# Kernel optimization log

Measured on AMD Instinct MI355X. Metric: run time of the kernel, lower is better.

The kernel has to match this reference:

```python
import jax, jax.numpy as jnp
import numpy as np

NUM_GROUPS = 8
EPS = 1e-5


def group_norm(x, gamma, beta):
    # x: [B, C, H, W]
    B, C, H, W = x.shape
    xg = x.reshape(B, NUM_GROUPS, C // NUM_GROUPS, H, W)
    mean = xg.mean(axis=(2, 3, 4), keepdims=True)
    var = xg.var(axis=(2, 3, 4), keepdims=True)
    xn = ((xg - mean) * jax.lax.rsqrt(var + EPS)).reshape(B, C, H, W)
    return xn * gamma[None, :, None, None] + beta[None, :, None, None]


def conv1x1(x, w, b):
    # x: [B, C, H, W], w: [Cout, Cin], b: [Cout]
    return jnp.einsum('bchw,oc->bohw', x, w) + b[None, :, None, None]


def setup_inputs() -> dict:
    key = jax.random.key(0)
    ks = jax.random.split(key, 7)
    C = 128
    x = jax.random.normal(ks[0], (4, C, 64, 64), dtype=jnp.float32)
    norm_w = jnp.ones((C,), dtype=jnp.float32)
    norm_b = jnp.zeros((C,), dtype=jnp.float32)
    s = 1.0 / np.sqrt(C)
    qkv_w = jax.random.normal(ks[1], (3 * C, C), dtype=jnp.float32) * s
    qkv_b = jax.random.normal(ks[2], (3 * C,), dtype=jnp.float32) * 0.01
    proj_w = jax.random.normal(ks[3], (C, C), dtype=jnp.float32) * s
    proj_b = jax.random.normal(ks[4], (C,), dtype=jnp.float32) * 0.01
    return {"x": x, "norm_w": norm_w, "norm_b": norm_b,
            "qkv_w": qkv_w, "qkv_b": qkv_b,
            "proj_w": proj_w, "proj_b": proj_b}


def reference(x, norm_w, norm_b, qkv_w, qkv_b, proj_w, proj_b):
    B, C, H, W = x.shape
    qkv = conv1x1(group_norm(x, norm_w, norm_b), qkv_w, qkv_b)
    q, k, v = jnp.split(qkv, 3, axis=1)           # each [B, C, H, W]
    q = q.reshape(B, C, H * W).transpose(0, 2, 1)  # [B, HW, C]
    k = k.reshape(B, C, H * W)                     # [B, C, HW]
    v = v.reshape(B, C, H * W).transpose(0, 2, 1)  # [B, HW, C]
    scale = 1.0 / np.sqrt(C).astype(np.float32)
    attn = jax.nn.softmax(jnp.einsum('bnc,bcm->bnm', q, k) * scale, axis=-1)
    out = jnp.einsum('bnm,bmc->bnc', attn, v)      # [B, HW, C]
    out = out.transpose(0, 2, 1).reshape(B, C, H, W)
    return x + conv1x1(out, proj_w, proj_b)
```

## Files before the change

kernel.cpp:

```cpp
#include <hip/hip_runtime.h>

typedef unsigned short u16;
typedef unsigned int   u32;

#define HW 4096
#define NC 128

typedef __bf16 bf16x8 __attribute__((ext_vector_type(8)));
typedef float  f32x16 __attribute__((ext_vector_type(16)));

__device__ __forceinline__ bf16x8 as_bf8(uint4 u){
    union { uint4 u; bf16x8 b; } c; c.u = u; return c.b;
}
__device__ __forceinline__ u16 f2bf(float f){
    u32 u = __float_as_uint(f);
    return (u16)((u + 0x7fffu + ((u >> 16) & 1u)) >> 16);
}
__device__ __forceinline__ u32 pack2(float a, float b){
    return ((__float_as_uint(a) + 0x8000u) >> 16) | ((__float_as_uint(b) + 0x8000u) & 0xffff0000u);
}
__device__ __forceinline__ float bf_lo(u32 u){ return __uint_as_float(u << 16); }
__device__ __forceinline__ float bf_hi(u32 u){ return __uint_as_float(u & 0xffff0000u); }
__device__ __forceinline__ void unpack8(uint4 u, float* v){
    v[0]=bf_lo(u.x); v[1]=bf_hi(u.x); v[2]=bf_lo(u.y); v[3]=bf_hi(u.y);
    v[4]=bf_lo(u.z); v[5]=bf_hi(u.z); v[6]=bf_lo(u.w); v[7]=bf_hi(u.w);
}

#define GLOAD_LDS16(g, l) \
    __builtin_amdgcn_global_load_lds((const __attribute__((address_space(1))) u32*)(const void*)(g), \
                                     (__attribute__((address_space(3))) u32*)(void*)(l), 16, 0, 0)

__global__ __launch_bounds__(256) void gn_stats_kernel(const float* __restrict__ x,
                                                       float* __restrict__ stats){
    int bg = blockIdx.x >> 3, part = blockIdx.x & 7;
    const float4* p = (const float4*)(x + (size_t)bg * 65536 + part * 8192);
    float s = 0.f, ss = 0.f;
    #pragma unroll
    for (int i = 0; i < 8; i++){
        float4 u = p[threadIdx.x + i*256];
        s  += u.x + u.y + u.z + u.w;
        ss += u.x*u.x + u.y*u.y + u.z*u.z + u.w*u.w;
    }
    #pragma unroll
    for (int off = 32; off > 0; off >>= 1){
        s  += __shfl_xor(s,  off);
        ss += __shfl_xor(ss, off);
    }
    __shared__ float rs[4], rss[4];
    int wid = threadIdx.x >> 6;
    if ((threadIdx.x & 63) == 0){ rs[wid] = s; rss[wid] = ss; }
    __syncthreads();
    if (threadIdx.x == 0){
        stats[bg*16 + part*2]     = rs[0]+rs[1]+rs[2]+rs[3];
        stats[bg*16 + part*2 + 1] = rss[0]+rss[1]+rss[2]+rss[3];
    }
}

__global__ __launch_bounds__(256) void wprep_kernel(const float* __restrict__ qkv_w,
                                                    const float* __restrict__ proj_w,
                                                    uint4* __restrict__ Wf,
                                                    uint4* __restrict__ Pf){
    int id = blockIdx.x*256 + threadIdx.x;
    const float* src; uint4* dst; int fi;
    if (id < 6144){ src = qkv_w; dst = Wf; fi = id; }
    else          { src = proj_w; dst = Pf; fi = id - 6144; }
    int l = fi & 63, ks = (fi >> 6) & 7, ob = fi >> 9;
    int o = ob*32 + (l & 31);
    int c = ks*16 + ((l >> 5) << 3);
    const float* s = src + o*128 + c;
    dst[fi] = make_uint4(pack2(s[0],s[1]), pack2(s[2],s[3]), pack2(s[4],s[5]), pack2(s[6],s[7]));
}

__global__ __launch_bounds__(256) void qkv_kernel(const float* __restrict__ x,
                                                  const float* __restrict__ stats,
                                                  const float* __restrict__ gamma,
                                                  const float* __restrict__ beta,
                                                  const uint4* __restrict__ Wf,
                                                  const float* __restrict__ bias,
                                                  uint4* __restrict__ Qf,
                                                  uint4* __restrict__ Kf,
                                                  uint4* __restrict__ Vf){
    __shared__ float gaL[128], beL[128], biasL[384];
    int b = blockIdx.x >> 7, tokblk = blockIdx.x & 127;
    int t = threadIdx.x, lane = t & 63, wv = t >> 6;
    if (t < 128){
        int g = t >> 4;
        float S = 0.f, SS = 0.f;
        #pragma unroll
        for (int p = 0; p < 8; p++){
            S  += stats[(b*8 + g)*16 + p*2];
            SS += stats[(b*8 + g)*16 + p*2 + 1];
        }
        float mean = S * (1.f/65536.f);
        float rstd = rsqrtf(SS * (1.f/65536.f) - mean*mean + 1e-5f);
        float ga = gamma[t] * rstd;
        gaL[t] = ga; beL[t] = beta[t] - mean*ga;
    }
    if (t < 192){ biasL[t] = bias[t]; biasL[t+192] = bias[t+192]; }
    __syncthreads();

    int h = lane >> 5, tl = lane & 31;
    uint4 xf[8];
    const float* xb = x + (size_t)b*128*HW + tokblk*32 + tl;
    #pragma unroll
    for (int ks = 0; ks < 8; ks++){
        int c0 = ks*16 + h*8;
        float4 g0 = *(float4*)&gaL[c0], g1 = *(float4*)&gaL[c0+4];
        float4 e0 = *(float4*)&beL[c0], e1 = *(float4*)&beL[c0+4];
        float v[8];
        #pragma unroll
        for (int j = 0; j < 8; j++) v[j] = xb[(size_t)(c0+j)*HW];
        v[0] = fmaf(v[0], g0.x, e0.x); v[1] = fmaf(v[1], g0.y, e0.y);
        v[2] = fmaf(v[2], g0.z, e0.z); v[3] = fmaf(v[3], g0.w, e0.w);
        v[4] = fmaf(v[4], g1.x, e1.x); v[5] = fmaf(v[5], g1.y, e1.y);
        v[6] = fmaf(v[6], g1.z, e1.z); v[7] = fmaf(v[7], g1.w, e1.w);
        xf[ks] = make_uint4(pack2(v[0],v[1]), pack2(v[2],v[3]), pack2(v[4],v[5]), pack2(v[6],v[7]));
    }

    bool up = (lane >= 32);
    #pragma unroll
    for (int i = 0; i < 3; i++){
        int ob = wv*3 + i;
        uint4 wf[8];
        #pragma unroll
        for (int ks = 0; ks < 8; ks++) wf[ks] = Wf[(ob*8 + ks)*64 + lane];
        f32x16 D;
        #pragma unroll
        for (int r = 0; r < 16; r++) D[r] = 0.f;
        if (ob < 8){
            #pragma unroll
            for (int ks = 0; ks < 8; ks++)
                D = __builtin_amdgcn_mfma_f32_32x32x16_bf16(as_bf8(wf[ks]), as_bf8(xf[ks]), D, 0,0,0);
            #pragma unroll
            for (int r = 0; r < 16; r++)
                D[r] += biasL[ob*32 + (r&3) + 8*(r>>2) + 4*h];
            u32 pk[8], xch[8];
            #pragma unroll
            for (int j = 0; j < 8; j++) pk[j] = pack2(D[2*j], D[2*j+1]);
            #pragma unroll
            for (int j = 0; j < 8; j++) xch[j] = __shfl_xor(pk[j], 32);
            uint4 F0 = up ? make_uint4(xch[2],xch[3],pk[2],pk[3]) : make_uint4(pk[0],pk[1],xch[0],xch[1]);
            uint4 F1 = up ? make_uint4(xch[6],xch[7],pk[6],pk[7]) : make_uint4(pk[4],pk[5],xch[4],xch[5]);
            uint4* dst = (ob < 4) ? Qf : Kf;
            int obl = ob & 3;
            size_t base = (((size_t)b*128 + tokblk)*8 + obl*2)*64 + lane;
            dst[base] = F0; dst[base + 64] = F1;
        } else {
            #pragma unroll
            for (int ks = 0; ks < 8; ks++)
                D = __builtin_amdgcn_mfma_f32_32x32x16_bf16(as_bf8(xf[ks]), as_bf8(wf[ks]), D, 0,0,0);
            int nb = ob - 8;
            float vb = biasL[256 + nb*32 + tl];
            #pragma unroll
            for (int r = 0; r < 16; r++) D[r] += vb;
            u32 pk[8], xch[8];
            #pragma unroll
            for (int j = 0; j < 8; j++) pk[j] = pack2(D[2*j], D[2*j+1]);
            #pragma unroll
            for (int j = 0; j < 8; j++) xch[j] = __shfl_xor(pk[j], 32);
            uint4 F0 = up ? make_uint4(xch[2],xch[3],pk[2],pk[3]) : make_uint4(pk[0],pk[1],xch[0],xch[1]);
            uint4 F1 = up ? make_uint4(xch[6],xch[7],pk[6],pk[7]) : make_uint4(pk[4],pk[5],xch[4],xch[5]);
            int it = tokblk >> 1, t2 = tokblk & 1;
            size_t base = ((((size_t)b*64 + it)*4 + nb)*4 + t2*2)*64 + lane;
            Vf[base] = F0; Vf[base + 64] = F1;
        }
    }
}

__global__ __launch_bounds__(256, 2) void attn_kernel(const uint4* __restrict__ Qf,
                                                      const uint4* __restrict__ Kf,
                                                      const uint4* __restrict__ Vf,
                                                      u16* __restrict__ Opart,
                                                      float* __restrict__ lsum){
    __shared__ uint4 smem[4096];
    int pair = blockIdx.x & 7, qx = blockIdx.x >> 3;
    int b = pair >> 1, ksp = pair & 1;
    int t = threadIdx.x, lane = t & 63, wv = t >> 6;
    int qh = wv >> 1, kh = wv & 1;
    const float SC = 0.08838834764831845f;

    uint4 qf[8];
    const uint4* qptr = Qf + ((size_t)b*128 + qx*2 + qh)*512 + lane;
    #pragma unroll
    for (int ks = 0; ks < 8; ks++) qf[ks] = qptr[ks*64];

    f32x16 O0, O1, O2, O3;
    #pragma unroll
    for (int r = 0; r < 16; r++){ O0[r]=0.f; O1[r]=0.f; O2[r]=0.f; O3[r]=0.f; }
    float l_i = 0.f;

    const uint4* kg = Kf + ((size_t)b*128 + ksp*64)*512;
    const uint4* vg = Vf + ((size_t)b*64  + ksp*32)*1024;

    #pragma unroll
    for (int i = 0; i < 4; i++){
        GLOAD_LDS16(kg + t + i*256, &smem[t + i*256]);
        GLOAD_LDS16(vg + t + i*256, &smem[2048 + t + i*256]);
    }
    __syncthreads();

    for (int it = 0; it < 32; it++){
        int cur = it & 1;
        if (it < 31){
            const uint4* kg2 = kg + (it+1)*1024;
            const uint4* vg2 = vg + (it+1)*1024;
            #pragma unroll
            for (int i = 0; i < 4; i++){
                GLOAD_LDS16(kg2 + t + i*256, &smem[(cur^1)*1024 + t + i*256]);
                GLOAD_LDS16(vg2 + t + i*256, &smem[2048 + (cur^1)*1024 + t + i*256]);
            }
        }

        f32x16 S0;
        #pragma unroll
        for (int r = 0; r < 16; r++) S0[r] = 0.f;
        #pragma unroll
        for (int ks = 0; ks < 8; ks++)
            S0 = __builtin_amdgcn_mfma_f32_32x32x16_bf16(
                     as_bf8(smem[cur*1024 + ((kh*8 + ks)<<6) + lane]),
                     as_bf8(qf[ks]), S0, 0,0,0);

        float psum = 0.f;
        u32 pk[8];
        #pragma unroll
        for (int q = 0; q < 4; q++){
            float e0 = __expf(__fmaf_rn(S0[q*4+0], SC, -8.f));
            float e1 = __expf(__fmaf_rn(S0[q*4+1], SC, -8.f));
            float e2 = __expf(__fmaf_rn(S0[q*4+2], SC, -8.f));
            float e3 = __expf(__fmaf_rn(S0[q*4+3], SC, -8.f));
            psum += (e0+e1)+(e2+e3);
            pk[2*q] = pack2(e0,e1); pk[2*q+1] = pack2(e2,e3);
        }
        psum += __shfl_xor(psum, 32);
        l_i += psum;

        u32 xch[8];
        #pragma unroll
        for (int i = 0; i < 8; i++) xch[i] = __shfl_xor(pk[i], 32);
        bool up = (lane >= 32);
        uint4 fr0 = up ? make_uint4(xch[2],xch[3],pk[2],pk[3]) : make_uint4(pk[0],pk[1],xch[0],xch[1]);
        uint4 fr1 = up ? make_uint4(xch[6],xch[7],pk[6],pk[7]) : make_uint4(pk[4],pk[5],xch[4],xch[5]);

        int vb = 2048 + cur*1024 + (kh<<7);
        #pragma unroll
        for (int ks = 0; ks < 2; ks++){
            bf16x8 pa = as_bf8(ks ? fr1 : fr0);
            O0 = __builtin_amdgcn_mfma_f32_32x32x16_bf16(pa, as_bf8(smem[vb +   0 + (ks<<6) + lane]), O0, 0,0,0);
            O1 = __builtin_amdgcn_mfma_f32_32x32x16_bf16(pa, as_bf8(smem[vb + 256 + (ks<<6) + lane]), O1, 0,0,0);
            O2 = __builtin_amdgcn_mfma_f32_32x32x16_bf16(pa, as_bf8(smem[vb + 512 + (ks<<6) + lane]), O2, 0,0,0);
            O3 = __builtin_amdgcn_mfma_f32_32x32x16_bf16(pa, as_bf8(smem[vb + 768 + (ks<<6) + lane]), O3, 0,0,0);
        }
        __syncthreads();
    }

    float* fsm  = (float*)smem;
    float* lred = fsm + 8192;
    if (kh == 1){
        #pragma unroll
        for (int r = 0; r < 16; r++){
            fsm[((qh*4+0)*16 + r)*64 + lane] = O0[r];
            fsm[((qh*4+1)*16 + r)*64 + lane] = O1[r];
            fsm[((qh*4+2)*16 + r)*64 + lane] = O2[r];
            fsm[((qh*4+3)*16 + r)*64 + lane] = O3[r];
        }
        if (lane < 32) lred[qh*32 + lane] = l_i;
    }
    __syncthreads();
    if (kh == 0){
        float lt = l_i + lred[qh*32 + (lane & 31)];
        if (lane < 32) lsum[((size_t)(ksp*4 + b))*HW + qx*64 + qh*32 + lane] = lt;
        u16* ob = Opart + (((size_t)(ksp*4 + b))*HW + qx*64 + qh*32)*NC;
        #pragma unroll
        for (int r = 0; r < 16; r++){
            int qr = (r&3) + 8*(r>>2) + 4*(lane>>5);
            int c  = lane & 31;
            ob[qr*NC +      c] = f2bf(O0[r] + fsm[((qh*4+0)*16 + r)*64 + lane]);
            ob[qr*NC + 32 + c] = f2bf(O1[r] + fsm[((qh*4+1)*16 + r)*64 + lane]);
            ob[qr*NC + 64 + c] = f2bf(O2[r] + fsm[((qh*4+2)*16 + r)*64 + lane]);
            ob[qr*NC + 96 + c] = f2bf(O3[r] + fsm[((qh*4+3)*16 + r)*64 + lane]);
        }
    }
}

__global__ __launch_bounds__(256) void combine_kernel(const u16* __restrict__ Op,
                                                      const float* __restrict__ lsum,
                                                      uint4* __restrict__ ao){
    int idx = blockIdx.x*256 + threadIdx.x;
    int row = idx >> 4, cg = idx & 15;
    float inv = 1.f / (lsum[row] + lsum[16384 + row]);
    uint4 u0 = *(const uint4*)(Op + (size_t)row*NC + cg*8);
    uint4 u1 = *(const uint4*)(Op + (size_t)2097152 + (size_t)row*NC + cg*8);
    float v0[8], v1[8];
    unpack8(u0, v0); unpack8(u1, v1);
    u32 pk[4];
    #pragma unroll
    for (int j = 0; j < 4; j++){
        float r0 = (v0[2*j]   + v1[2*j])   * inv;
        float r1 = (v0[2*j+1] + v1[2*j+1]) * inv;
        pk[j] = pack2(r0, r1);
    }
    size_t fi = (((size_t)(row >> 5))*8 + (cg >> 1))*64 + (row & 31) + ((cg & 1) << 5);
    ao[fi] = make_uint4(pk[0], pk[1], pk[2], pk[3]);
}

__global__ __launch_bounds__(256) void proj_kernel(const uint4* __restrict__ aof,
                                                   const uint4* __restrict__ Pf,
                                                   const float* __restrict__ bias,
                                                   const float* __restrict__ x,
                                                   float* __restrict__ out){
    __shared__ float biasL[128];
    int t = threadIdx.x, lane = t & 63, wv = t >> 6;
    if (t < 128) biasL[t] = bias[t];
    __syncthreads();
    int b = blockIdx.x >> 6, tk = blockIdx.x & 63;
    int tokb2 = wv & 1, obh = wv >> 1;
    int tokblk = tk*2 + tokb2;
    int h = lane >> 5, tl = lane & 31;

    uint4 af[8];
    const uint4* ab = aof + (((size_t)b*128 + tokblk)*8)*64 + lane;
    #pragma unroll
    for (int ks = 0; ks < 8; ks++) af[ks] = ab[ks*64];

    #pragma unroll
    for (int i = 0; i < 2; i++){
        int ob = obh*2 + i;
        uint4 pf[8];
        #pragma unroll
        for (int ks = 0; ks < 8; ks++) pf[ks] = Pf[(ob*8 + ks)*64 + lane];
        f32x16 D;
        #pragma unroll
        for (int r = 0; r < 16; r++) D[r] = 0.f;
        #pragma unroll
        for (int ks = 0; ks < 8; ks++)
            D = __builtin_amdgcn_mfma_f32_32x32x16_bf16(as_bf8(pf[ks]), as_bf8(af[ks]), D, 0,0,0);
        #pragma unroll
        for (int r = 0; r < 16; r++){
            int o = ob*32 + (r&3) + 8*(r>>2) + 4*h;
            size_t gi = ((size_t)b*128 + o)*HW + tokblk*32 + tl;
            out[gi] = x[gi] + biasL[o] + D[r];
        }
    }
}

extern "C" void kernel_launch(void* const* d_in, const int* in_sizes, int n_in,
                              void* d_out, int out_size, void* d_ws, size_t ws_size,
                              hipStream_t stream){
    const float* x      = (const float*)d_in[0];
    const float* norm_w = (const float*)d_in[1];
    const float* norm_b = (const float*)d_in[2];
    const float* qkv_w  = (const float*)d_in[3];
    const float* qkv_b  = (const float*)d_in[4];
    const float* proj_w = (const float*)d_in[5];
    const float* proj_b = (const float*)d_in[6];
    float* out = (float*)d_out;

    char* w = (char*)d_ws;
    float* stats = (float*)w;
    uint4* Qf = (uint4*)(w + 2048);
    uint4* Kf = (uint4*)(w + 2048 + 4194304);
    uint4* Vf = (uint4*)(w + 2048 + 8388608);
    float* lsum = (float*)(w + 2048 + 12582912);
    uint4* Wf = (uint4*)(w + 2048 + 12582912 + 131072);
    uint4* Pf = (uint4*)(w + 2048 + 12582912 + 131072 + 98304);
    uint4* ao = Qf;
    u16* Opart = (u16*)d_out;

    gn_stats_kernel<<<256, 256, 0, stream>>>(x, stats);
    wprep_kernel<<<32, 256, 0, stream>>>(qkv_w, proj_w, Wf, Pf);
    qkv_kernel<<<512, 256, 0, stream>>>(x, stats, norm_w, norm_b, Wf, qkv_b, Qf, Kf, Vf);
    attn_kernel<<<512, 256, 0, stream>>>(Qf, Kf, Vf, Opart, lsum);
    combine_kernel<<<1024, 256, 0, stream>>>(Opart, lsum, ao);
    proj_kernel<<<256, 256, 0, stream>>>(ao, Pf, proj_b, x, out);
}
```

Measured before the change: 147.5 us.

## Fuse prep kernels, fold combine into proj, load V to registers in attention

Merges the group-norm stats and weight-prep kernels into one launch, removes the separate combine kernel by having the projection kernel sum the two split-K partial outputs and normalize by lsum on load, and changes attention to read V fragments directly from global into registers instead of staging them in LDS. This cuts launch count and an intermediate buffer round-trip, and halves attention LDS usage. It risks less coalesced partial-output reads in proj and more global V traffic per wave in attention.

```diff
diff --git a/kernel.cpp b/kernel.cpp
--- a/kernel.cpp
+++ b/kernel.cpp
@@ -30,45 +30,46 @@
     __builtin_amdgcn_global_load_lds((const __attribute__((address_space(1))) u32*)(const void*)(g), \
                                      (__attribute__((address_space(3))) u32*)(void*)(l), 16, 0, 0)
 
-__global__ __launch_bounds__(256) void gn_stats_kernel(const float* __restrict__ x,
-                                                       float* __restrict__ stats){
-    int bg = blockIdx.x >> 3, part = blockIdx.x & 7;
-    const float4* p = (const float4*)(x + (size_t)bg * 65536 + part * 8192);
-    float s = 0.f, ss = 0.f;
-    #pragma unroll
-    for (int i = 0; i < 8; i++){
-        float4 u = p[threadIdx.x + i*256];
-        s  += u.x + u.y + u.z + u.w;
-        ss += u.x*u.x + u.y*u.y + u.z*u.z + u.w*u.w;
-    }
-    #pragma unroll
-    for (int off = 32; off > 0; off >>= 1){
-        s  += __shfl_xor(s,  off);
-        ss += __shfl_xor(ss, off);
-    }
-    __shared__ float rs[4], rss[4];
-    int wid = threadIdx.x >> 6;
-    if ((threadIdx.x & 63) == 0){ rs[wid] = s; rss[wid] = ss; }
-    __syncthreads();
-    if (threadIdx.x == 0){
-        stats[bg*16 + part*2]     = rs[0]+rs[1]+rs[2]+rs[3];
-        stats[bg*16 + part*2 + 1] = rss[0]+rss[1]+rss[2]+rss[3];
-    }
-}
-
-__global__ __launch_bounds__(256) void wprep_kernel(const float* __restrict__ qkv_w,
-                                                    const float* __restrict__ proj_w,
-                                                    uint4* __restrict__ Wf,
-                                                    uint4* __restrict__ Pf){
-    int id = blockIdx.x*256 + threadIdx.x;
-    const float* src; uint4* dst; int fi;
-    if (id < 6144){ src = qkv_w; dst = Wf; fi = id; }
-    else          { src = proj_w; dst = Pf; fi = id - 6144; }
-    int l = fi & 63, ks = (fi >> 6) & 7, ob = fi >> 9;
-    int o = ob*32 + (l & 31);
-    int c = ks*16 + ((l >> 5) << 3);
-    const float* s = src + o*128 + c;
-    dst[fi] = make_uint4(pack2(s[0],s[1]), pack2(s[2],s[3]), pack2(s[4],s[5]), pack2(s[6],s[7]));
+__global__ __launch_bounds__(256) void gnw_kernel(const float* __restrict__ x,
+                                                  float* __restrict__ stats,
+                                                  const float* __restrict__ qkv_w,
+                                                  const float* __restrict__ proj_w,
+                                                  uint4* __restrict__ Wf,
+                                                  uint4* __restrict__ Pf){
+    if (blockIdx.x < 256){
+        int bg = blockIdx.x >> 3, part = blockIdx.x & 7;
+        const float4* p = (const float4*)(x + (size_t)bg * 65536 + part * 8192);
+        float s = 0.f, ss = 0.f;
+        #pragma unroll
+        for (int i = 0; i < 8; i++){
+            float4 u = p[threadIdx.x + i*256];
+            s  += u.x + u.y + u.z + u.w;
+            ss += u.x*u.x + u.y*u.y + u.z*u.z + u.w*u.w;
+        }
+        #pragma unroll
+        for (int off = 32; off > 0; off >>= 1){
+            s  += __shfl_xor(s,  off);
+            ss += __shfl_xor(ss, off);
+        }
+        __shared__ float rs[4], rss[4];
+        int wid = threadIdx.x >> 6;
+        if ((threadIdx.x & 63) == 0){ rs[wid] = s; rss[wid] = ss; }
+        __syncthreads();
+        if (threadIdx.x == 0){
+            stats[bg*16 + part*2]     = rs[0]+rs[1]+rs[2]+rs[3];
+            stats[bg*16 + part*2 + 1] = rss[0]+rss[1]+rss[2]+rss[3];
+        }
+    } else {
+        int id = (blockIdx.x - 256)*256 + threadIdx.x;
+        const float* src; uint4* dst; int fi;
+        if (id < 6144){ src = qkv_w; dst = Wf; fi = id; }
+        else          { src = proj_w; dst = Pf; fi = id - 6144; }
+        int l = fi & 63, ks = (fi >> 6) & 7, ob = fi >> 9;
+        int o = ob*32 + (l & 31);
+        int c = ks*16 + ((l >> 5) << 3);
+        const float* s = src + o*128 + c;
+        dst[fi] = make_uint4(pack2(s[0],s[1]), pack2(s[2],s[3]), pack2(s[4],s[5]), pack2(s[6],s[7]));
+    }
 }
 
 __global__ __launch_bounds__(256) void qkv_kernel(const float* __restrict__ x,
@@ -172,7 +173,8 @@
                                                       const uint4* __restrict__ Vf,
                                                       u16* __restrict__ Opart,
                                                       float* __restrict__ lsum){
-    __shared__ uint4 smem[4096];
+    __shared__ uint4 smem[2048];
+    __shared__ float lred[64];
     int pair = blockIdx.x & 7, qx = blockIdx.x >> 3;
     int b = pair >> 1, ksp = pair & 1;
     int t = threadIdx.x, lane = t & 63, wv = t >> 6;
@@ -193,22 +195,24 @@
     const uint4* vg = Vf + ((size_t)b*64  + ksp*32)*1024;
 
     #pragma unroll
-    for (int i = 0; i < 4; i++){
+    for (int i = 0; i < 4; i++)
         GLOAD_LDS16(kg + t + i*256, &smem[t + i*256]);
-        GLOAD_LDS16(vg + t + i*256, &smem[2048 + t + i*256]);
-    }
     __syncthreads();
 
     for (int it = 0; it < 32; it++){
         int cur = it & 1;
         if (it < 31){
             const uint4* kg2 = kg + (it+1)*1024;
-            const uint4* vg2 = vg + (it+1)*1024;
-            #pragma unroll
-            for (int i = 0; i < 4; i++){
+            #pragma unroll
+            for (int i = 0; i < 4; i++)
                 GLOAD_LDS16(kg2 + t + i*256, &smem[(cur^1)*1024 + t + i*256]);
-                GLOAD_LDS16(vg2 + t + i*256, &smem[2048 + (cur^1)*1024 + t + i*256]);
-            }
+        }
+        const uint4* vgi = vg + it*1024 + lane;
+        uint4 vf[8];
+        #pragma unroll
+        for (int nb = 0; nb < 4; nb++){
+            vf[nb*2]   = vgi[(nb*4 + kh*2)     << 6];
+            vf[nb*2+1] = vgi[(nb*4 + kh*2 + 1) << 6];
         }
 
         f32x16 S0;
@@ -241,20 +245,18 @@
         uint4 fr0 = up ? make_uint4(xch[2],xch[3],pk[2],pk[3]) : make_uint4(pk[0],pk[1],xch[0],xch[1]);
         uint4 fr1 = up ? make_uint4(xch[6],xch[7],pk[6],pk[7]) : make_uint4(pk[4],pk[5],xch[4],xch[5]);
 
-        int vb = 2048 + cur*1024 + (kh<<7);
         #pragma unroll
         for (int ks = 0; ks < 2; ks++){
             bf16x8 pa = as_bf8(ks ? fr1 : fr0);
-            O0 = __builtin_amdgcn_mfma_f32_32x32x16_bf16(pa, as_bf8(smem[vb +   0 + (ks<<6) + lane]), O0, 0,0,0);
-            O1 = __builtin_amdgcn_mfma_f32_32x32x16_bf16(pa, as_bf8(smem[vb + 256 + (ks<<6) + lane]), O1, 0,0,0);
-            O2 = __builtin_amdgcn_mfma_f32_32x32x16_bf16(pa, as_bf8(smem[vb + 512 + (ks<<6) + lane]), O2, 0,0,0);
-            O3 = __builtin_amdgcn_mfma_f32_32x32x16_bf16(pa, as_bf8(smem[vb + 768 + (ks<<6) + lane]), O3, 0,0,0);
+            O0 = __builtin_amdgcn_mfma_f32_32x32x16_bf16(pa, as_bf8(vf[0*2+ks]), O0, 0,0,0);
+            O1 = __builtin_amdgcn_mfma_f32_32x32x16_bf16(pa, as_bf8(vf[1*2+ks]), O1, 0,0,0);
+            O2 = __builtin_amdgcn_mfma_f32_32x32x16_bf16(pa, as_bf8(vf[2*2+ks]), O2, 0,0,0);
+            O3 = __builtin_amdgcn_mfma_f32_32x32x16_bf16(pa, as_bf8(vf[3*2+ks]), O3, 0,0,0);
         }
         __syncthreads();
     }
 
-    float* fsm  = (float*)smem;
-    float* lred = fsm + 8192;
+    float* fsm = (float*)smem;
     if (kh == 1){
         #pragma unroll
         for (int r = 0; r < 16; r++){
@@ -282,28 +284,8 @@
     }
 }
 
-__global__ __launch_bounds__(256) void combine_kernel(const u16* __restrict__ Op,
-                                                      const float* __restrict__ lsum,
-                                                      uint4* __restrict__ ao){
-    int idx = blockIdx.x*256 + threadIdx.x;
-    int row = idx >> 4, cg = idx & 15;
-    float inv = 1.f / (lsum[row] + lsum[16384 + row]);
-    uint4 u0 = *(const uint4*)(Op + (size_t)row*NC + cg*8);
-    uint4 u1 = *(const uint4*)(Op + (size_t)2097152 + (size_t)row*NC + cg*8);
-    float v0[8], v1[8];
-    unpack8(u0, v0); unpack8(u1, v1);
-    u32 pk[4];
-    #pragma unroll
-    for (int j = 0; j < 4; j++){
-        float r0 = (v0[2*j]   + v1[2*j])   * inv;
-        float r1 = (v0[2*j+1] + v1[2*j+1]) * inv;
-        pk[j] = pack2(r0, r1);
-    }
-    size_t fi = (((size_t)(row >> 5))*8 + (cg >> 1))*64 + (row & 31) + ((cg & 1) << 5);
-    ao[fi] = make_uint4(pk[0], pk[1], pk[2], pk[3]);
-}
-
-__global__ __launch_bounds__(256) void proj_kernel(const uint4* __restrict__ aof,
+__global__ __launch_bounds__(256) void proj_kernel(const u16* __restrict__ Op,
+                                                   const float* __restrict__ lsum,
                                                    const uint4* __restrict__ Pf,
                                                    const float* __restrict__ bias,
                                                    const float* __restrict__ x,
@@ -317,10 +299,22 @@
     int tokblk = tk*2 + tokb2;
     int h = lane >> 5, tl = lane & 31;
 
+    int rowg = b*HW + tokblk*32 + tl;
+    float inv = 1.f / (lsum[rowg] + lsum[16384 + rowg]);
+    const u16* p0 = Op + (size_t)rowg*NC + h*8;
     uint4 af[8];
-    const uint4* ab = aof + (((size_t)b*128 + tokblk)*8)*64 + lane;
-    #pragma unroll
-    for (int ks = 0; ks < 8; ks++) af[ks] = ab[ks*64];
+    #pragma unroll
+    for (int ks = 0; ks < 8; ks++){
+        uint4 u0 = *(const uint4*)(p0 + ks*16);
+        uint4 u1 = *(const uint4*)(p0 + 2097152 + ks*16);
+        float v0[8], v1[8];
+        unpack8(u0, v0); unpack8(u1, v1);
+        u32 q[4];
+        #pragma unroll
+        for (int j = 0; j < 4; j++)
+            q[j] = pack2((v0[2*j] + v1[2*j]) * inv, (v0[2*j+1] + v1[2*j+1]) * inv);
+        af[ks] = make_uint4(q[0], q[1], q[2], q[3]);
+    }
 
     #pragma unroll
     for (int i = 0; i < 2; i++){
@@ -363,13 +357,10 @@
     float* lsum = (float*)(w + 2048 + 12582912);
     uint4* Wf = (uint4*)(w + 2048 + 12582912 + 131072);
     uint4* Pf = (uint4*)(w + 2048 + 12582912 + 131072 + 98304);
-    uint4* ao = Qf;
     u16* Opart = (u16*)d_out;
 
-    gn_stats_kernel<<<256, 256, 0, stream>>>(x, stats);
-    wprep_kernel<<<32, 256, 0, stream>>>(qkv_w, proj_w, Wf, Pf);
+    gnw_kernel<<<288, 256, 0, stream>>>(x, stats, qkv_w, proj_w, Wf, Pf);
     qkv_kernel<<<512, 256, 0, stream>>>(x, stats, norm_w, norm_b, Wf, qkv_b, Qf, Kf, Vf);
     attn_kernel<<<512, 256, 0, stream>>>(Qf, Kf, Vf, Opart, lsum);
-    combine_kernel<<<1024, 256, 0, stream>>>(Opart, lsum, ao);
-    proj_kernel<<<256, 256, 0, stream>>>(ao, Pf, proj_b, x, out);
-}
+    proj_kernel<<<256, 256, 0, stream>>>(Opart, lsum, Pf, proj_b, x, out);
+}
```

Result: faster. 141.0 us (-4.5%).
